# Kernel tuning notes

Hardware: AMD Instinct MI355X
Metric: run time of the kernel (lower is better)

Reference implementation:

```python
import jax, jax.numpy as jnp
import numpy as np

K = 3
STRIDE = 1
PADDING = 1


def _conv2d(x, w, b, stride, padding):
    out = jax.lax.conv_general_dilated(
        x, w, window_strides=(stride, stride),
        padding=[(padding, padding), (padding, padding)],
        dimension_numbers=('NCHW', 'OIHW', 'NCHW'))
    return out + b[None, :, None, None]


def _grid_sample_bilinear_zeros(x, grid):
    B, C, Hin, Win = x.shape
    gx = (grid[..., 0] + 1.0) * (Win * 0.5) - 0.5  # (B,Hg,Wg) pixel coords
    gy = (grid[..., 1] + 1.0) * (Hin * 0.5) - 0.5
    x0f = jnp.floor(gx)
    y0f = jnp.floor(gy)
    wx1 = gx - x0f  # bilinear weights
    wy1 = gy - y0f
    x0 = x0f.astype(jnp.int32)
    y0 = y0f.astype(jnp.int32)
    xf = x.reshape(B, C, Hin * Win)

    def gather(yi, xi):
        valid = (xi >= 0) & (xi < Win) & (yi >= 0) & (yi < Hin)  # zero padding
        idx = jnp.clip(yi, 0, Hin - 1) * Win + jnp.clip(xi, 0, Win - 1)
        g = jax.vmap(lambda xb, ib: xb[:, ib])(xf, idx)  # (B,C,Hg,Wg)
        return g * valid[:, None, :, :].astype(x.dtype)

    w00 = ((1.0 - wx1) * (1.0 - wy1))[:, None]
    w01 = (wx1 * (1.0 - wy1))[:, None]
    w10 = ((1.0 - wx1) * wy1)[:, None]
    w11 = (wx1 * wy1)[:, None]
    return (gather(y0, x0) * w00 + gather(y0, x0 + 1) * w01 +
            gather(y0 + 1, x0) * w10 + gather(y0 + 1, x0 + 1) * w11)


def setup_inputs() -> dict:
    key = jax.random.key(0)
    k1, k2, k3 = jax.random.split(key, 3)
    B, C, O, H, W = 8, 128, 128, 64, 64
    x = jax.random.normal(k1, (B, C, H, W), dtype=jnp.float32)
    # small offset-predictor weights so sampled locations stay near the grid
    w_off = jax.random.normal(k2, (2 * K * K, C, K, K), dtype=jnp.float32) * 1e-3
    b_off = jnp.zeros((2 * K * K,), dtype=jnp.float32)
    w_main = jax.random.normal(k3, (O, C, K, K), dtype=jnp.float32) * 0.05
    b_main = jnp.zeros((O,), dtype=jnp.float32)
    return {"x": x, "w_off": w_off, "b_off": b_off, "w_main": w_main, "b_main": b_main}


def reference(x, w_off, b_off, w_main, b_main):
    offset = _conv2d(x, w_off, b_off, STRIDE, PADDING)  # (B, 2*K*K, H, W)
    B, _, H, W = offset.shape
    off = jnp.transpose(offset, (0, 2, 3, 1)).reshape(B, H, W, K, K, 2)
    # The torch in-place loops reduce to:
    #   x-comp: cumsum over i of column j=0, broadcast over j
    #   y-comp: cumsum over j of row    i=0, broadcast over i
    ox = jnp.cumsum(off[:, :, :, :, 0, 0], axis=3)  # (B,H,W,K)
    oy = jnp.cumsum(off[:, :, :, 0, :, 1], axis=3)  # (B,H,W,K)
    ox_f = jnp.broadcast_to(ox[..., None], (B, H, W, K, K))
    oy_f = jnp.broadcast_to(oy[:, :, :, None, :], (B, H, W, K, K))
    off_f = jnp.stack([ox_f, oy_f], axis=-1).reshape(B, H, W, K * K, 2)

    y_range = jnp.linspace(-1.0, 1.0, H, dtype=x.dtype)
    x_range = jnp.linspace(-1.0, 1.0, W, dtype=x.dtype)
    yg, xg = jnp.meshgrid(y_range, x_range, indexing='ij')
    base = jnp.stack((xg, yg), axis=-1)  # (H,W,2)
    grid = base[None, :, :, None, :] + off_f  # (B,H,W,K*K,2)
    grid = grid.reshape(B, H, W * K * K, 2)

    xs = _grid_sample_bilinear_zeros(x, grid)  # (B,C,H,W*K*K)
    C = x.shape[1]
    xs = xs.reshape(B, C, H, W, K * K)
    wm = w_main.reshape(w_main.shape[0], C, K * K)
    out = jnp.einsum('bchwk,ock->bohw', xs, wm)
    return out + b_main[None, :, None, None]
```

## Files before the change

kernel.cpp:

```cpp
#include <hip/hip_runtime.h>
#include <hip/hip_bf16.h>
#include <stdint.h>

typedef unsigned short u16;
typedef unsigned int u32;
typedef __attribute__((ext_vector_type(8))) short short8;
typedef __attribute__((ext_vector_type(4))) float float4v;
typedef __attribute__((ext_vector_type(2))) float float2v;

#define CH 128
#define OO 128
#define KD 1152
#define MPIX 32768
#define LDBp 136

#define BAR_LDS() do { \
    asm volatile("s_waitcnt lgkmcnt(0)" ::: "memory"); \
    __builtin_amdgcn_s_barrier(); \
} while (0)

__device__ __forceinline__ u16 f2bf(float v) {
    __hip_bfloat16 h = __float2bfloat16(v);
    return *reinterpret_cast<u16*>(&h);
}

__device__ __forceinline__ float bf_lo(u32 u) {
    u32 t = u << 16;
    return __builtin_bit_cast(float, t);
}
__device__ __forceinline__ float bf_hi(u32 u) {
    u32 t = u & 0xffff0000u;
    return __builtin_bit_cast(float, t);
}
__device__ __forceinline__ float2v unpk(u32 u) {
    float2v r;
    r.x = bf_lo(u);
    r.y = bf_hi(u);
    return r;
}
__device__ __forceinline__ u32 pack_bf16(float lo, float hi) {
    return (u32)f2bf(lo) | ((u32)f2bf(hi) << 16);
}

__global__ __launch_bounds__(256) void prep_kernel(const float* __restrict__ x,
                                                   const float* __restrict__ w_off,
                                                   const float* __restrict__ w_main,
                                                   __hip_bfloat16* __restrict__ xt,
                                                   float* __restrict__ partial,
                                                   u16* __restrict__ Wb) {
    __shared__ float st[64][65];
    int tid = threadIdx.x;
    int bid = blockIdx.x;

    if (bid < 512) {
        int bh = bid;
        int b = bh >> 6;
        int h = bh & 63;
        const float* xb = x + ((size_t)b * CH) * 4096 + (size_t)h * 64;
        u32* xo32 = (u32*)(xt + ((size_t)bh << 6) * CH);
        for (int cc0 = 0; cc0 < 128; cc0 += 64) {
            #pragma unroll
            for (int step = 0; step < 16; ++step) {
                int cl = (tid >> 6) + step * 4;
                int w = tid & 63;
                st[cl][w] = xb[(size_t)(cc0 + cl) * 4096 + w];
            }
            __syncthreads();
            #pragma unroll
            for (int step = 0; step < 8; ++step) {
                int w = (tid >> 5) + step * 8;
                int p = tid & 31;
                u32 pair = pack_bf16(st[2 * p][w], st[2 * p + 1][w]);
                xo32[(size_t)w * 64 + (cc0 >> 1) + p] = pair;
            }
            __syncthreads();
        }
    } else if (bid < 1024) {
        int idx = bid - 512;
        int m = (idx & 127) * 256 + tid;
        int chunk = idx >> 7;
        int b = m >> 12;
        int hw = m & 4095;
        int h = hw >> 6;
        int w = hw & 63;
        float acc[6] = {0.f, 0.f, 0.f, 0.f, 0.f, 0.f};
        int c0 = chunk * 32;
        for (int c = c0; c < c0 + 32; ++c) {
            const float* xc = x + ((size_t)(b * CH + c) << 12);
            float xv[9];
            #pragma unroll
            for (int dy = 0; dy < 3; ++dy) {
                int yy = h + dy - 1;
                bool vy = (unsigned)yy < 64u;
                #pragma unroll
                for (int dx = 0; dx < 3; ++dx) {
                    int xx = w + dx - 1;
                    bool vv = vy && ((unsigned)xx < 64u);
                    xv[dy * 3 + dx] = vv ? xc[yy * 64 + xx] : 0.f;
                }
            }
            const float* wb = w_off + (size_t)c * 9;
            #pragma unroll
            for (int s = 0; s < 6; ++s) {
                int chn = (s < 3) ? s * 6 : (s - 3) * 2 + 1;
                const float* wp = wb + (size_t)chn * (CH * 9);
                float a = acc[s];
                #pragma unroll
                for (int t = 0; t < 9; ++t) a = fmaf(xv[t], wp[t], a);
                acc[s] = a;
            }
        }
        float* po = partial + ((size_t)(chunk << 15) + m) * 6;
        #pragma unroll
        for (int s = 0; s < 6; ++s) po[s] = acc[s];
    } else {
        int idx = (bid - 1024) * 256 + tid;
        if (idx < OO * KD) {
            int o = idx / KD;
            int r = idx - o * KD;
            int k = r >> 7;
            int c = r & 127;
            Wb[idx] = f2bf(w_main[(size_t)o * KD + c * 9 + k]);
        }
    }
}

__global__ __launch_bounds__(256, 2) void fused_gemm_kernel(const __hip_bfloat16* __restrict__ xt,
                                                            const float* __restrict__ partial,
                                                            const float* __restrict__ b_off,
                                                            const u16* __restrict__ Wb,
                                                            const float* __restrict__ b_main,
                                                            float* __restrict__ out) {
    __shared__ float offs[64][6];
    __shared__ __align__(16) float4v twt[64][9];
    __shared__ __align__(16) int4 tbs[64][9];
    __shared__ __align__(16) u16 lA[2][128 * 32];
    __shared__ __align__(16) u16 lB[2][64 * LDBp];

    int tid = threadIdx.x;
    int orig = blockIdx.x;
    int b = orig & 7;
    int h = orig >> 3;
    int m0 = ((b << 6) + h) << 6;

    for (int idx = tid; idx < 64 * 6; idx += 256) {
        int pix = idx / 6, s = idx % 6;
        int m = m0 + pix;
        int chn = (s < 3) ? s * 6 : (s - 3) * 2 + 1;
        float v = b_off[chn];
        #pragma unroll
        for (int q = 0; q < 4; ++q) v += partial[((size_t)(q << 15) + m) * 6 + s];
        offs[pix][s] = v;
    }
    __syncthreads();

    for (int i2 = tid; i2 < 64 * 9; i2 += 256) {
        int pix = i2 / 9, k = i2 % 9;
        int i = k / 3, j = k - i * 3;
        float ox = offs[pix][0];
        if (i >= 1) ox += offs[pix][1];
        if (i >= 2) ox += offs[pix][2];
        float oy = offs[pix][3];
        if (j >= 1) oy += offs[pix][4];
        if (j >= 2) oy += offs[pix][5];
        const float step = 2.0f / 63.0f;
        float bxn = -1.0f + pix * step;
        float byn = -1.0f + h * step;
        float gx = fmaf(bxn + ox, 32.0f, 31.5f);
        float gy = fmaf(byn + oy, 32.0f, 31.5f);
        float x0f = floorf(gx), y0f = floorf(gy);
        float wx = gx - x0f, wy = gy - y0f;
        int ix0 = (int)x0f, iy0 = (int)y0f;
        int ix1 = ix0 + 1, iy1 = iy0 + 1;
        float fx0 = ((unsigned)ix0 < 64u) ? 1.f : 0.f;
        float fx1 = ((unsigned)ix1 < 64u) ? 1.f : 0.f;
        float fy0 = ((unsigned)iy0 < 64u) ? 1.f : 0.f;
        float fy1 = ((unsigned)iy1 < 64u) ? 1.f : 0.f;
        float4v wv;
        wv[0] = (1.f - wy) * (1.f - wx) * fy0 * fx0;
        wv[1] = (1.f - wy) * wx * fy0 * fx1;
        wv[2] = wy * (1.f - wx) * fy1 * fx0;
        wv[3] = wy * wx * fy1 * fx1;
        int cx0 = min(max(ix0, 0), 63), cx1 = min(max(ix1, 0), 63);
        int cy0 = min(max(iy0, 0), 63), cy1 = min(max(iy1, 0), 63);
        twt[pix][k] = wv;
        tbs[pix][k] = make_int4((cy0 * 64 + cx0) * 64, (cy0 * 64 + cx1) * 64,
                                (cy1 * 64 + cx0) * 64, (cy1 * 64 + cx1) * 64);
    }
    __syncthreads();

    int wave = tid >> 6, lane = tid & 63;
    int wo = wave & 1;
    int wp = wave >> 1;
    int mrow = lane & 15;
    int q8 = (lane >> 4) * 8;

    int ar = tid >> 2;
    int ag = (tid & 3) * 8;
    const u16* aptr0 = Wb + (size_t)ar * KD + ag;
    const u16* aptr1 = aptr0 + (size_t)64 * KD;
    int asto = ar * 32 + ag;

    int pixB = tid >> 2;
    int t4 = tid & 3;
    int t4o = t4 * 4;
    const u32* xb = (const u32*)(xt + (((size_t)b << 12) * (size_t)CH));
    int bwb = pixB * LDBp + t4 * 8;

    float4v acc[4][2];
    #pragma unroll
    for (int sm = 0; sm < 4; ++sm)
        #pragma unroll
        for (int sn = 0; sn < 2; ++sn)
            acc[sm][sn] = (float4v){0.f, 0.f, 0.f, 0.f};

    float4v wv;
    int4 bv;
    uint4 u[4][4];

    auto burst = [&](int t) {
        wv = twt[pixB][t];
        bv = tbs[pixB][t];
        #pragma unroll
        for (int q = 0; q < 4; ++q) {
            u[0][q] = *(const uint4*)(xb + bv.x + q * 16 + t4o);
            u[1][q] = *(const uint4*)(xb + bv.y + q * 16 + t4o);
            u[2][q] = *(const uint4*)(xb + bv.z + q * 16 + t4o);
            u[3][q] = *(const uint4*)(xb + bv.w + q * 16 + t4o);
        }
    };

    auto blendq = [&](const uint4& a0, const uint4& a1, const uint4& a2,
                      const uint4& a3, int col, u16* lBw) {
        const u32* p00 = (const u32*)&a0;
        const u32* p01 = (const u32*)&a1;
        const u32* p10 = (const u32*)&a2;
        const u32* p11 = (const u32*)&a3;
        u32 outp[4];
        #pragma unroll
        for (int j = 0; j < 4; ++j) {
            float2v p = unpk(p00[j]) * wv[0];
            p += unpk(p01[j]) * wv[1];
            p += unpk(p10[j]) * wv[2];
            p += unpk(p11[j]) * wv[3];
            outp[j] = pack_bf16(p.x, p.y);
        }
        *(uint4*)&lBw[bwb + col] = *(const uint4*)outp;
    };

    auto stepA = [&](int kk, uint4& c0, uint4& c1, uint4& n0, uint4& n1, u16* lAc) {
        *(uint4*)&lAc[asto] = c0;
        *(uint4*)&lAc[asto + 64 * 32] = c1;
        if (kk + 1 < 36) {
            n0 = *(const uint4*)(aptr0 + (size_t)(kk + 1) * 32);
            n1 = *(const uint4*)(aptr1 + (size_t)(kk + 1) * 32);
        }
    };

    auto mfma_step = [&](const u16* lAc, const u16* lBr, int col) {
        short8 af[4], bfv[2];
        #pragma unroll
        for (int i = 0; i < 4; ++i)
            af[i] = *(const short8*)&lAc[(wo * 64 + i * 16 + mrow) * 32 + q8];
        #pragma unroll
        for (int sn = 0; sn < 2; ++sn)
            bfv[sn] = *(const short8*)&lBr[(wp * 32 + sn * 16 + mrow) * LDBp + col + q8];
        #pragma unroll
        for (int i = 0; i < 4; ++i)
            #pragma unroll
            for (int sn = 0; sn < 2; ++sn)
                acc[i][sn] = __builtin_amdgcn_mfma_f32_16x16x32_bf16(af[i], bfv[sn],
                                                                    acc[i][sn], 0, 0, 0);
    };

    uint4 aC0 = *(const uint4*)aptr0;
    uint4 aC1 = *(const uint4*)aptr1;
    uint4 aN0, aN1;
    burst(0);
    {
        u16* lBw = &lB[0][0];
        blendq(u[0][0], u[1][0], u[2][0], u[3][0], 0,  lBw);
        blendq(u[0][1], u[1][1], u[2][1], u[3][1], 32, lBw);
        blendq(u[0][2], u[1][2], u[2][2], u[3][2], 64, lBw);
        blendq(u[0][3], u[1][3], u[2][3], u[3][3], 96, lBw);
    }

    for (int t = 0; t < 9; ++t) {
        int kk = t * 4;
        const u16* lBr = &lB[t & 1][0];
        u16* lBw = &lB[(t + 1) & 1][0];
        u16* lA0 = &lA[0][0];
        u16* lA1 = &lA[1][0];
        bool more = t < 8;

        if (more) burst(t + 1);
        stepA(kk, aC0, aC1, aN0, aN1, lA0);
        BAR_LDS();
        mfma_step(lA0, lBr, 0);

        stepA(kk + 1, aN0, aN1, aC0, aC1, lA1);
        BAR_LDS();
        mfma_step(lA1, lBr, 32);

        stepA(kk + 2, aC0, aC1, aN0, aN1, lA0);
        if (more) {
            blendq(u[0][0], u[1][0], u[2][0], u[3][0], 0,  lBw);
            blendq(u[0][1], u[1][1], u[2][1], u[3][1], 32, lBw);
        }
        BAR_LDS();
        mfma_step(lA0, lBr, 64);

        stepA(kk + 3, aN0, aN1, aC0, aC1, lA1);
        if (more) {
            blendq(u[0][2], u[1][2], u[2][2], u[3][2], 64, lBw);
            blendq(u[0][3], u[1][3], u[2][3], u[3][3], 96, lBw);
        }
        BAR_LDS();
        mfma_step(lA1, lBr, 96);
    }

    #pragma unroll
    for (int sm = 0; sm < 4; ++sm) {
        int o = wo * 64 + sm * 16 + (lane >> 4) * 4;
        #pragma unroll
        for (int sn = 0; sn < 2; ++sn) {
            int pcol = m0 + wp * 32 + sn * 16 + mrow;
            int rem = pcol & 4095;
            float* op = out + (((size_t)b * OO) << 12) + rem;
            #pragma unroll
            for (int r = 0; r < 4; ++r)
                op[(size_t)(o + r) << 12] = acc[sm][sn][r] + b_main[o + r];
        }
    }
}

extern "C" void kernel_launch(void* const* d_in, const int* in_sizes, int n_in,
                              void* d_out, int out_size, void* d_ws, size_t ws_size,
                              hipStream_t stream) {
    const float* x      = (const float*)d_in[0];
    const float* w_off  = (const float*)d_in[1];
    const float* b_off  = (const float*)d_in[2];
    const float* w_main = (const float*)d_in[3];
    const float* b_main = (const float*)d_in[4];
    float* out = (float*)d_out;

    char* ws = (char*)d_ws;
    __hip_bfloat16* xt = (__hip_bfloat16*)ws;
    float* partial = (float*)(ws + 8388608);
    u16* Wb   = (u16*)(ws + 8388608 + 3145728);

    prep_kernel<<<1600, 256, 0, stream>>>(x, w_off, w_main, xt, partial, Wb);
    fused_gemm_kernel<<<MPIX / 64, 256, 0, stream>>>(xt, partial, b_off, Wb, b_main, out);
}
```

Before: 126.1 us.

## Widen weight K-step to 64 with XOR-swizzled LDS and fewer barriers

Each weight staging step in the fused GEMM now covers 64 K elements instead of 32. The A tile in LDS uses an XOR swizzle to avoid bank conflicts, and the per-tap loop drops from four barriers to two. Gather base offsets are packed into one u32 per tap and decoded on the fly, which shrinks LDS use. The cost is more A registers in flight, a larger lA buffer, and blending all four B quarters before a single barrier, which may reduce overlap or occupancy.

```diff
diff --git a/kernel.cpp b/kernel.cpp
--- a/kernel.cpp
+++ b/kernel.cpp
@@ -13,6 +13,8 @@
 #define KD 1152
 #define MPIX 32768
 #define LDBp 136
+
+#define LDA_SW(row, col) ((row) * 64 + ((col) ^ (((row) & 7) << 3)))
 
 #define BAR_LDS() do { \
     asm volatile("s_waitcnt lgkmcnt(0)" ::: "memory"); \
@@ -133,8 +135,8 @@
                                                             float* __restrict__ out) {
     __shared__ float offs[64][6];
     __shared__ __align__(16) float4v twt[64][9];
-    __shared__ __align__(16) int4 tbs[64][9];
-    __shared__ __align__(16) u16 lA[2][128 * 32];
+    __shared__ u32 tbs[64][9];
+    __shared__ __align__(16) u16 lA[2][128 * 64];
     __shared__ __align__(16) u16 lB[2][64 * LDBp];
 
     int tid = threadIdx.x;
@@ -184,8 +186,7 @@
         int cx0 = min(max(ix0, 0), 63), cx1 = min(max(ix1, 0), 63);
         int cy0 = min(max(iy0, 0), 63), cy1 = min(max(iy1, 0), 63);
         twt[pix][k] = wv;
-        tbs[pix][k] = make_int4((cy0 * 64 + cx0) * 64, (cy0 * 64 + cx1) * 64,
-                                (cy1 * 64 + cx0) * 64, (cy1 * 64 + cx1) * 64);
+        tbs[pix][k] = (u32)cx0 | ((u32)cy0 << 8) | ((u32)cx1 << 16) | ((u32)cy1 << 24);
     }
     __syncthreads();
 
@@ -199,7 +200,6 @@
     int ag = (tid & 3) * 8;
     const u16* aptr0 = Wb + (size_t)ar * KD + ag;
     const u16* aptr1 = aptr0 + (size_t)64 * KD;
-    int asto = ar * 32 + ag;
 
     int pixB = tid >> 2;
     int t4 = tid & 3;
@@ -215,18 +215,23 @@
             acc[sm][sn] = (float4v){0.f, 0.f, 0.f, 0.f};
 
     float4v wv;
-    int4 bv;
     uint4 u[4][4];
 
     auto burst = [&](int t) {
         wv = twt[pixB][t];
-        bv = tbs[pixB][t];
+        u32 pc = tbs[pixB][t];
+        int cx0 = pc & 255, cy0 = (pc >> 8) & 255;
+        int cx1 = (pc >> 16) & 255, cy1 = (pc >> 24) & 255;
+        int b00 = ((cy0 << 6) + cx0) << 6;
+        int b01 = ((cy0 << 6) + cx1) << 6;
+        int b10 = ((cy1 << 6) + cx0) << 6;
+        int b11 = ((cy1 << 6) + cx1) << 6;
         #pragma unroll
         for (int q = 0; q < 4; ++q) {
-            u[0][q] = *(const uint4*)(xb + bv.x + q * 16 + t4o);
-            u[1][q] = *(const uint4*)(xb + bv.y + q * 16 + t4o);
-            u[2][q] = *(const uint4*)(xb + bv.z + q * 16 + t4o);
-            u[3][q] = *(const uint4*)(xb + bv.w + q * 16 + t4o);
+            u[0][q] = *(const uint4*)(xb + b00 + q * 16 + t4o);
+            u[1][q] = *(const uint4*)(xb + b01 + q * 16 + t4o);
+            u[2][q] = *(const uint4*)(xb + b10 + q * 16 + t4o);
+            u[3][q] = *(const uint4*)(xb + b11 + q * 16 + t4o);
         }
     };
 
@@ -248,34 +253,49 @@
         *(uint4*)&lBw[bwb + col] = *(const uint4*)outp;
     };
 
-    auto stepA = [&](int kk, uint4& c0, uint4& c1, uint4& n0, uint4& n1, u16* lAc) {
-        *(uint4*)&lAc[asto] = c0;
-        *(uint4*)&lAc[asto + 64 * 32] = c1;
-        if (kk + 1 < 36) {
-            n0 = *(const uint4*)(aptr0 + (size_t)(kk + 1) * 32);
-            n1 = *(const uint4*)(aptr1 + (size_t)(kk + 1) * 32);
+    auto stageA = [&](int kk, uint4& c0, uint4& c1, uint4& c2, uint4& c3,
+                      uint4& n0, uint4& n1, uint4& n2, uint4& n3, u16* lAc) {
+        *(uint4*)&lAc[LDA_SW(ar, ag)]           = c0;
+        *(uint4*)&lAc[LDA_SW(ar, ag + 32)]      = c1;
+        *(uint4*)&lAc[LDA_SW(ar + 64, ag)]      = c2;
+        *(uint4*)&lAc[LDA_SW(ar + 64, ag + 32)] = c3;
+        if (kk + 1 < 18) {
+            const u16* p0 = aptr0 + (size_t)(kk + 1) * 64;
+            const u16* p1 = aptr1 + (size_t)(kk + 1) * 64;
+            n0 = *(const uint4*)(p0);
+            n1 = *(const uint4*)(p0 + 32);
+            n2 = *(const uint4*)(p1);
+            n3 = *(const uint4*)(p1 + 32);
         }
     };
 
-    auto mfma_step = [&](const u16* lAc, const u16* lBr, int col) {
-        short8 af[4], bfv[2];
-        #pragma unroll
-        for (int i = 0; i < 4; ++i)
-            af[i] = *(const short8*)&lAc[(wo * 64 + i * 16 + mrow) * 32 + q8];
-        #pragma unroll
-        for (int sn = 0; sn < 2; ++sn)
-            bfv[sn] = *(const short8*)&lBr[(wp * 32 + sn * 16 + mrow) * LDBp + col + q8];
-        #pragma unroll
-        for (int i = 0; i < 4; ++i)
+    auto mfma_step = [&](const u16* lAc, const u16* lBr, int colB) {
+        #pragma unroll
+        for (int p = 0; p < 2; ++p) {
+            short8 af[4], bfv[2];
+            #pragma unroll
+            for (int i = 0; i < 4; ++i) {
+                int row = wo * 64 + i * 16 + mrow;
+                af[i] = *(const short8*)&lAc[LDA_SW(row, p * 32 + q8)];
+            }
             #pragma unroll
             for (int sn = 0; sn < 2; ++sn)
-                acc[i][sn] = __builtin_amdgcn_mfma_f32_16x16x32_bf16(af[i], bfv[sn],
-                                                                    acc[i][sn], 0, 0, 0);
+                bfv[sn] = *(const short8*)&lBr[(wp * 32 + sn * 16 + mrow) * LDBp +
+                                               colB + p * 32 + q8];
+            #pragma unroll
+            for (int i = 0; i < 4; ++i)
+                #pragma unroll
+                for (int sn = 0; sn < 2; ++sn)
+                    acc[i][sn] = __builtin_amdgcn_mfma_f32_16x16x32_bf16(af[i], bfv[sn],
+                                                                        acc[i][sn], 0, 0, 0);
+        }
     };
 
-    uint4 aC0 = *(const uint4*)aptr0;
-    uint4 aC1 = *(const uint4*)aptr1;
-    uint4 aN0, aN1;
+    uint4 aC0 = *(const uint4*)(aptr0);
+    uint4 aC1 = *(const uint4*)(aptr0 + 32);
+    uint4 aC2 = *(const uint4*)(aptr1);
+    uint4 aC3 = *(const uint4*)(aptr1 + 32);
+    uint4 aN0, aN1, aN2, aN3;
     burst(0);
     {
         u16* lBw = &lB[0][0];
@@ -286,7 +306,7 @@
     }
 
     for (int t = 0; t < 9; ++t) {
-        int kk = t * 4;
+        int kk = t * 2;
         const u16* lBr = &lB[t & 1][0];
         u16* lBw = &lB[(t + 1) & 1][0];
         u16* lA0 = &lA[0][0];
@@ -294,29 +314,19 @@
         bool more = t < 8;
 
         if (more) burst(t + 1);
-        stepA(kk, aC0, aC1, aN0, aN1, lA0);
+        stageA(kk, aC0, aC1, aC2, aC3, aN0, aN1, aN2, aN3, lA0);
         BAR_LDS();
         mfma_step(lA0, lBr, 0);
 
-        stepA(kk + 1, aN0, aN1, aC0, aC1, lA1);
-        BAR_LDS();
-        mfma_step(lA1, lBr, 32);
-
-        stepA(kk + 2, aC0, aC1, aN0, aN1, lA0);
+        stageA(kk + 1, aN0, aN1, aN2, aN3, aC0, aC1, aC2, aC3, lA1);
         if (more) {
             blendq(u[0][0], u[1][0], u[2][0], u[3][0], 0,  lBw);
             blendq(u[0][1], u[1][1], u[2][1], u[3][1], 32, lBw);
-        }
-        BAR_LDS();
-        mfma_step(lA0, lBr, 64);
-
-        stepA(kk + 3, aN0, aN1, aC0, aC1, lA1);
-        if (more) {
             blendq(u[0][2], u[1][2], u[2][2], u[3][2], 64, lBw);
             blendq(u[0][3], u[1][3], u[2][3], u[3][3], 96, lBw);
         }
         BAR_LDS();
-        mfma_step(lA1, lBr, 96);
+        mfma_step(lA1, lBr, 64);
     }
 
     #pragma unroll
```

Result: no change. 125.1 us (-0.8%).
